# Optimization experiments

Measured on AMD Instinct MI355X. Metric: run time of the kernel, lower is better.

The kernel has to match this reference:

```python
import jax, jax.numpy as jnp
import numpy as np

# PCEN constants (from __init__ defaults)
ALPHA = 0.98
DELTA = 2.0
R = 0.5
S = 0.025
EPS = 1e-6


def setup_inputs() -> dict:
    key = jax.random.key(0)
    # mel spectrogram energies: [batch, mel_bins, time], nonnegative
    x = jax.random.uniform(key, (64, 128, 4096), dtype=jnp.float32)
    return {"x": x}


def _ema_smooth(x):
    # x: [B, C, T]. smooth[0] = x[0]; smooth[t] = (1-S)*smooth[t-1] + S*x[t]
    x_t = jnp.moveaxis(x, -1, 0)  # [T, B, C]
    init = x_t[0]

    def step(carry, xt):
        sm = (1.0 - S) * carry + S * xt
        return sm, sm

    _, rest = jax.lax.scan(step, init, x_t[1:])  # [T-1, B, C]
    smooth = jnp.concatenate([init[None], rest], axis=0)  # [T, B, C]
    return jnp.moveaxis(smooth, 0, -1)  # [B, C, T]


def reference(x):
    smooth = _ema_smooth(x)
    return (x / (smooth + EPS) ** ALPHA + DELTA) ** R - DELTA ** R
```

## Files before the change

### kernel.cpp

```cpp
#include <hip/hip_runtime.h>
#include <math.h>


#define T_LEN 4096
#define BLOCK 256
#define PER   16

__global__ __launch_bounds__(BLOCK) void pcen_kernel(const float* __restrict__ x,
                                                     float* __restrict__ out) {
    constexpr float A_COEF = 0.975f;
    constexpr float S_COEF = 0.025f;
    constexpr float ALPHA  = 0.98f;
    constexpr float EPS    = 1e-6f;
    constexpr float DELTA  = 2.0f;
    constexpr float SQRT_DELTA = 1.4142135623730951f;

    const int row = blockIdx.x;
    const float* __restrict__ xr  = x   + (size_t)row * T_LEN;
    float* __restrict__       orr = out + (size_t)row * T_LEN;

    const int tid  = threadIdx.x;
    const int base = tid * PER;

    float xv[PER];
    const float4* xr4 = (const float4*)(xr + base);
#pragma unroll
    for (int i = 0; i < 4; ++i) {
        float4 v = xr4[i];
        xv[4*i+0] = v.x; xv[4*i+1] = v.y; xv[4*i+2] = v.z; xv[4*i+3] = v.w;
    }

    float A = 1.0f, B = 0.0f;
#pragma unroll
    for (int i = 0; i < PER; ++i) {
        float a = A_COEF, b = S_COEF * xv[i];
        if (base + i == 0) { a = 0.0f; b = xv[i]; }
        A = a * A;
        B = fmaf(a, B, b);
    }

    const int lane = tid & 63;
#pragma unroll
    for (int off = 1; off < 64; off <<= 1) {
        float Au = __shfl_up(A, off);
        float Bu = __shfl_up(B, off);
        if (lane >= off) {
            B = fmaf(A, Bu, B);
            A = A * Au;
        }
    }

    __shared__ float wA[BLOCK / 64], wB[BLOCK / 64];
    const int wid = tid >> 6;
    if (lane == 63) { wA[wid] = A; wB[wid] = B; }
    __syncthreads();

    float Aex = __shfl_up(A, 1);
    float Bex = __shfl_up(B, 1);
    if (lane == 0) { Aex = 1.0f; Bex = 0.0f; }

    float WA = 1.0f, WB = 0.0f;
    for (int w = 0; w < wid; ++w) {
        WB = fmaf(wA[w], WB, wB[w]);
        WA = wA[w] * WA;
    }

    float y = fmaf(Aex, WB, Bex);

    float ov[PER];
#pragma unroll
    for (int i = 0; i < PER; ++i) {
        if (base + i == 0) y = xv[i];
        else               y = fmaf(A_COEF, y, S_COEF * xv[i]);
        float p = __builtin_exp2f(-ALPHA * __builtin_log2f(y + EPS));
        ov[i] = sqrtf(fmaf(xv[i], p, DELTA)) - SQRT_DELTA;
    }

    float4* o4 = (float4*)(orr + base);
#pragma unroll
    for (int i = 0; i < 4; ++i) {
        float4 v;
        v.x = ov[4*i+0]; v.y = ov[4*i+1]; v.z = ov[4*i+2]; v.w = ov[4*i+3];
        o4[i] = v;
    }
}

extern "C" void kernel_launch(void* const* d_in, const int* in_sizes, int n_in,
                              void* d_out, int out_size, void* d_ws, size_t ws_size,
                              hipStream_t stream) {
    const float* x = (const float*)d_in[0];
    float* out = (float*)d_out;
    const int rows = in_sizes[0] / T_LEN;
    pcen_kernel<<<rows, BLOCK, 0, stream>>>(x, out);
}
```

Baseline: 234.1 us.

## Use 1024-thread blocks with 4 elements per thread and raw AMDGCN intrinsics

```diff
diff --git a/kernel.cpp b/kernel.cpp
--- a/kernel.cpp
+++ b/kernel.cpp
@@ -3,8 +3,9 @@
 
 
 #define T_LEN 4096
-#define BLOCK 256
-#define PER   16
+#define BLOCK 1024
+#define PER   4
+#define NWAVE (BLOCK / 64)
 
 __global__ __launch_bounds__(BLOCK) void pcen_kernel(const float* __restrict__ x,
                                                      float* __restrict__ out) {
@@ -23,20 +24,22 @@
     const int base = tid * PER;
 
     float xv[PER];
-    const float4* xr4 = (const float4*)(xr + base);
-#pragma unroll
-    for (int i = 0; i < 4; ++i) {
-        float4 v = xr4[i];
-        xv[4*i+0] = v.x; xv[4*i+1] = v.y; xv[4*i+2] = v.z; xv[4*i+3] = v.w;
+    {
+        float4 v = *(const float4*)(xr + base);
+        xv[0] = v.x; xv[1] = v.y; xv[2] = v.z; xv[3] = v.w;
     }
 
-    float A = 1.0f, B = 0.0f;
+    float A, B;
+    if (tid == 0) {
+        A = 0.0f; B = xv[0];
+        for (int i = 1; i < PER; ++i) { B = fmaf(A_COEF, B, S_COEF * xv[i]); }
+    } else {
+        A = A_COEF; B = S_COEF * xv[0];
 #pragma unroll
-    for (int i = 0; i < PER; ++i) {
-        float a = A_COEF, b = S_COEF * xv[i];
-        if (base + i == 0) { a = 0.0f; b = xv[i]; }
-        A = a * A;
-        B = fmaf(a, B, b);
+        for (int i = 1; i < PER; ++i) {
+            B = fmaf(A_COEF, B, S_COEF * xv[i]);
+            A = A * A_COEF;
+        }
     }
 
     const int lane = tid & 63;
@@ -50,7 +53,7 @@
         }
     }
 
-    __shared__ float wA[BLOCK / 64], wB[BLOCK / 64];
+    __shared__ float wA[NWAVE], wB[NWAVE];
     const int wid = tid >> 6;
     if (lane == 63) { wA[wid] = A; wB[wid] = B; }
     __syncthreads();
@@ -59,10 +62,9 @@
     float Bex = __shfl_up(B, 1);
     if (lane == 0) { Aex = 1.0f; Bex = 0.0f; }
 
-    float WA = 1.0f, WB = 0.0f;
+    float WB = 0.0f;
     for (int w = 0; w < wid; ++w) {
         WB = fmaf(wA[w], WB, wB[w]);
-        WA = wA[w] * WA;
     }
 
     float y = fmaf(Aex, WB, Bex);
@@ -70,19 +72,15 @@
     float ov[PER];
 #pragma unroll
     for (int i = 0; i < PER; ++i) {
-        if (base + i == 0) y = xv[i];
-        else               y = fmaf(A_COEF, y, S_COEF * xv[i]);
-        float p = __builtin_exp2f(-ALPHA * __builtin_log2f(y + EPS));
-        ov[i] = sqrtf(fmaf(xv[i], p, DELTA)) - SQRT_DELTA;
+        if (tid == 0 && i == 0) y = xv[0];
+        else                    y = fmaf(A_COEF, y, S_COEF * xv[i]);
+        float p = __builtin_amdgcn_exp2f(-ALPHA * __builtin_amdgcn_logf(y + EPS));
+        ov[i] = __builtin_amdgcn_sqrtf(fmaf(xv[i], p, DELTA)) - SQRT_DELTA;
     }
 
-    float4* o4 = (float4*)(orr + base);
-#pragma unroll
-    for (int i = 0; i < 4; ++i) {
-        float4 v;
-        v.x = ov[4*i+0]; v.y = ov[4*i+1]; v.z = ov[4*i+2]; v.w = ov[4*i+3];
-        o4[i] = v;
-    }
+    float4 v;
+    v.x = ov[0]; v.y = ov[1]; v.z = ov[2]; v.w = ov[3];
+    *(float4*)(orr + base) = v;
 }
 
 extern "C" void kernel_launch(void* const* d_in, const int* in_sizes, int n_in,
```

Measured after the change: 223.5 us. 4.5% less time.
